# Optimization experiments

Hardware: AMD Instinct MI355X
Metric: run time of the kernel (lower is better)

## Reference

```python
import jax, jax.numpy as jnp
import numpy as np

B, S, H, I, E, TOP_K = 2, 2048, 768, 3072, 7, 2


def setup_inputs() -> dict:
    key = jax.random.key(0)
    ks = jax.random.split(key, 5)
    x = jax.random.normal(ks[0], (B, S, H), dtype=jnp.float32)
    # parameter init ~ torch Linear default scale (1/sqrt(fan_in))
    wg = jax.random.normal(ks[1], (H, E), dtype=jnp.float32) / np.sqrt(H)
    bg = jnp.zeros((E,), dtype=jnp.float32)
    w1 = jax.random.normal(ks[2], (E, H, I), dtype=jnp.float32) / np.sqrt(H)
    b1 = jnp.zeros((E, I), dtype=jnp.float32)
    w2 = jax.random.normal(ks[3], (E, I, H), dtype=jnp.float32) / np.sqrt(I)
    b2 = jnp.zeros((E, H), dtype=jnp.float32)
    return {"x": x, "wg": wg, "bg": bg, "w1": w1, "b1": b1, "w2": w2, "b2": b2}


def _gate_weights(gate_logits):
    # top-k mask: -inf everywhere except top-k slots, then softmax.
    # Equivalent: softmax over top-k values, scattered back into [.., E].
    vals, idx = jax.lax.top_k(gate_logits, TOP_K)           # [B,S,K]
    wk = jax.nn.softmax(vals, axis=-1)                       # [B,S,K]
    onehot = jax.nn.one_hot(idx, E, dtype=gate_logits.dtype)  # [B,S,K,E]
    return jnp.einsum('bsk,bske->bse', wk, onehot)           # [B,S,E]


def reference(x, wg, bg, w1, b1, w2, b2):
    gate_logits = jnp.einsum('bsh,he->bse', x, wg) + bg      # [B,S,E]
    gate_w = _gate_weights(gate_logits)                       # [B,S,E]
    # dense all-expert FFN (the module evaluates EVERY expert on every token)
    h = jnp.einsum('bsh,ehi->bsei', x, w1) + b1              # [B,S,E,I]
    h = jax.nn.gelu(h, approximate=False)                    # torch.nn.GELU (exact erf)
    expert_out = jnp.einsum('bsei,eih->bseh', h, w2) + b2    # [B,S,E,H]
    out = jnp.einsum('bseh,bse->bsh', expert_out, gate_w)    # weighted combine
    # dropout is identity in eval mode
    return (out, gate_w)
```

## Files before the change

### kernel.cpp

```cpp
#include <hip/hip_runtime.h>
#include <hip/hip_bf16.h>
#include <cmath>

#define NT 4096
#define HD 768
#define ID 3072
#define NE 7
#define NP 8192
#define TM 128
#define TN 128
#define BK 32
#define KS 2
#define NT2 (HD / TN)
#define SLOTS 384
#define NRING 3

using short8 = __attribute__((ext_vector_type(8))) short;
using f32x4  = __attribute__((ext_vector_type(4))) float;
typedef __hip_bfloat16 bf16;

typedef const __attribute__((address_space(1))) void* gas_ptr;
typedef __attribute__((address_space(3))) void* las_ptr;
#define GLDS(g, l) __builtin_amdgcn_global_load_lds((gas_ptr)(g), (las_ptr)(l), 16, 0, 0)

#define BAR()   asm volatile("s_barrier" ::: "memory")
#define WAITL() asm volatile("s_waitcnt lgkmcnt(0)" ::: "memory")
#define WV4()   asm volatile("s_waitcnt vmcnt(4)" ::: "memory")
#define WV0()   asm volatile("s_waitcnt vmcnt(0)" ::: "memory")
#define SCHEDB() __builtin_amdgcn_sched_barrier(0)

__device__ inline float b2f(unsigned short u) {
  unsigned v = (unsigned)u << 16; float f; __builtin_memcpy(&f, &v, 4); return f;
}

__device__ inline float gelu_erf(float v) {
  float xa = fabsf(v) * 0.70710678118654752f;
  float t  = __builtin_amdgcn_rcpf(1.0f + 0.3275911f * xa);
  float p  = t * (0.254829592f + t * (-0.284496736f + t * (1.421413741f +
             t * (-1.453152027f + t * 1.061405429f))));
  float er = 1.0f - p * __expf(-xa * xa);
  er = (v < 0.0f) ? -er : er;
  return 0.5f * v * (1.0f + er);
}

__global__ __launch_bounds__(64) void gate_kernel(
    const float* __restrict__ x, const float* __restrict__ wg, const float* __restrict__ bg,
    float* __restrict__ gate_out, bf16* __restrict__ xb,
    float* __restrict__ pair_w, int* __restrict__ tokexp)
{
  int t = blockIdx.x;
  int lane = threadIdx.x;
  const float* xr = x + (size_t)t * HD;
  float acc[NE];
#pragma unroll
  for (int e = 0; e < NE; e++) acc[e] = 0.f;
#pragma unroll
  for (int j = 0; j < HD / 64; j++) {
    int h = lane + j * 64;
    float xv = xr[h];
    xb[(size_t)t * HD + h] = __float2bfloat16(xv);
    const float* wr = wg + (size_t)h * NE;
#pragma unroll
    for (int e = 0; e < NE; e++) acc[e] += xv * wr[e];
  }
#pragma unroll
  for (int e = 0; e < NE; e++) {
    float v = acc[e];
    for (int s = 32; s > 0; s >>= 1) v += __shfl_down(v, s, 64);
    acc[e] = v;
  }
  if (lane == 0) {
    float lg[NE];
#pragma unroll
    for (int e = 0; e < NE; e++) lg[e] = acc[e] + bg[e];
    int i0 = 0;
    for (int e = 1; e < NE; e++) if (lg[e] > lg[i0]) i0 = e;
    int i1 = -1;
    for (int e = 0; e < NE; e++) {
      if (e == i0) continue;
      if (i1 < 0 || lg[e] > lg[i1]) i1 = e;
    }
    float v0 = lg[i0], v1 = lg[i1];
    float e1 = expf(v1 - v0);
    float inv = 1.f / (1.f + e1);
    float w0 = inv, w1v = e1 * inv;
    float* go = gate_out + (size_t)t * NE;
#pragma unroll
    for (int e = 0; e < NE; e++) go[e] = 0.f;
    go[i0] = w0; go[i1] = w1v;
    pair_w[2 * t + 0] = w0;
    pair_w[2 * t + 1] = w1v;
    tokexp[2 * t + 0] = i0;
    tokexp[2 * t + 1] = i1;
  }
}

__global__ __launch_bounds__(256) void route_kernel(
    const int* __restrict__ tokexp, int* __restrict__ elist, int* __restrict__ counts)
{
  __shared__ int wcnt[4];
  int e = blockIdx.x;
  int tid = threadIdx.x, wv = tid >> 6, ln = tid & 63;
  int base = 0;
  for (int chunk = 0; chunk < NP; chunk += 256) {
    int p = chunk + tid;
    bool m = (tokexp[p] == e);
    unsigned long long bal = __ballot(m);
    if (ln == 0) wcnt[wv] = __popcll(bal);
    __syncthreads();
    int pre = 0;
#pragma unroll
    for (int w = 0; w < 4; w++) pre += (w < wv) ? wcnt[w] : 0;
    int rank = pre + __popcll(bal & ((1ull << ln) - 1ull));
    if (m) elist[e * NP + base + rank] = p;
    base += wcnt[0] + wcnt[1] + wcnt[2] + wcnt[3];
    __syncthreads();
  }
  if (tid == 0) counts[e] = base;
}

__global__ __launch_bounds__(256) void transpose_cvt_kernel(
    const float* __restrict__ src, bf16* __restrict__ dst, int K, int N)
{
  __shared__ float tile[64][65];
  int e = blockIdx.z;
  int n0 = blockIdx.x * 64;
  int k0 = blockIdx.y * 64;
  const float* s = src + (size_t)e * K * N;
  bf16* d = dst + (size_t)e * K * N;
  int t = threadIdx.x;
  {
    int kk = t >> 4;
    int nc = (t & 15) << 2;
#pragma unroll
    for (int r = 0; r < 4; r++) {
      int k = kk + r * 16;
      float4 v = *(const float4*)(s + (size_t)(k0 + k) * N + n0 + nc);
      tile[k][nc + 0] = v.x; tile[k][nc + 1] = v.y;
      tile[k][nc + 2] = v.z; tile[k][nc + 3] = v.w;
    }
  }
  __syncthreads();
  {
    int c = t & 15;
    int nbase = t >> 4;
#pragma unroll
    for (int r = 0; r < 4; r++) {
      int n = nbase + r * 16;
      bf16 tmp[4];
#pragma unroll
      for (int i = 0; i < 4; i++) tmp[i] = __float2bfloat16(tile[4 * c + i][n]);
      ushort4 u; __builtin_memcpy(&u, tmp, 8);
      *(ushort4*)(d + (size_t)(n0 + n) * K + k0 + 4 * c) = u;
    }
  }
}


#define STAGE_TILE(As_, Bs_, a0_, a1_, bA_, bB_, t_, s_, c0_, c1_) do {          \
    bf16* dA_ = (bf16*)(As_) + (size_t)(s_) * TM * 32;                           \
    bf16* dB_ = (bf16*)(Bs_) + (size_t)(s_) * TN * 32;                           \
    GLDS((a0_) + (size_t)(t_) * BK, dA_ + (c0_) * 8);                            \
    GLDS((a1_) + (size_t)(t_) * BK, dA_ + (c1_) * 8);                            \
    GLDS((bA_) + (size_t)(t_) * BK, dB_ + (c0_) * 8);                            \
    GLDS((bB_) + (size_t)(t_) * BK, dB_ + (c1_) * 8);                            \
  } while (0)

__global__ __launch_bounds__(256) void ffn1_kernel(
    const bf16* __restrict__ xb, const bf16* __restrict__ w1t, const float* __restrict__ b1,
    const int* __restrict__ counts, const int* __restrict__ elist, bf16* __restrict__ hbuf)
{
  __shared__ bf16 As[NRING][TM][4][8];
  __shared__ bf16 Bs[NRING][TN][4][8];
  __shared__ int plist[TM];

  int tid = threadIdx.x;
  int e, base = 0, cnt = 0, acct = 0;
  bool found = false;
  for (e = 0; e < NE; e++) {
    cnt = counts[e];
    int tiles = (cnt + TM - 1) / TM;
    if ((int)blockIdx.y < acct + tiles) { base = ((int)blockIdx.y - acct) * TM; found = true; break; }
    acct += tiles;
  }
  if (!found) return;

  if (tid < TM) {
    int r = base + tid;
    plist[tid] = (r < cnt) ? elist[e * NP + r] : -1;
  }
  __syncthreads();

  const int n0 = blockIdx.x * TN;
  const bf16* Bsrc = w1t + (size_t)e * ID * HD;

  int c0 = tid, c1 = tid + 256;
  int r0 = c0 >> 2, p0 = c0 & 3, k0 = p0 ^ ((r0 >> 1) & 3);
  int r1 = c1 >> 2, p1 = c1 & 3, k1 = p1 ^ ((r1 >> 1) & 3);
  int pr0 = plist[r0], pr1 = plist[r1];
  const bf16* a0 = xb + (size_t)((pr0 >= 0 ? pr0 : 0) >> 1) * HD + k0 * 8;
  const bf16* a1 = xb + (size_t)((pr1 >= 0 ? pr1 : 0) >> 1) * HD + k1 * 8;
  const bf16* b0 = Bsrc + (size_t)(n0 + r0) * HD + k0 * 8;
  const bf16* b1v = Bsrc + (size_t)(n0 + r1) * HD + k1 * 8;

  int wave = tid >> 6, lane = tid & 63;
  int wm = (wave & 1) << 6, wn = (wave >> 1) << 6;
  int lr = lane & 15, quad = lane >> 4;
  int ph = quad ^ ((lr >> 1) & 3);

  f32x4 acc[4][4] = {};
  const int NIT = HD / BK;

  STAGE_TILE(As, Bs, a0, a1, b0, b1v, 0, 0, c0, c1);
  STAGE_TILE(As, Bs, a0, a1, b0, b1v, 1, 1, c0, c1);

  int sr = 0;
  for (int t = 0; t < NIT; ++t) {
    if (t < NIT - 1) { WV4(); } else { WV0(); }
    BAR();
    short8 af[4], bfr[4];
#pragma unroll
    for (int i = 0; i < 4; i++) af[i] = *(const short8*)&As[sr][wm + i * 16 + lr][ph][0];
#pragma unroll
    for (int j = 0; j < 4; j++) bfr[j] = *(const short8*)&Bs[sr][wn + j * 16 + lr][ph][0];
    if (t + 2 < NIT) {
      int sw = sr + 2; if (sw >= NRING) sw -= NRING;
      STAGE_TILE(As, Bs, a0, a1, b0, b1v, t + 2, sw, c0, c1);
    }
    WAITL(); SCHEDB();
    __builtin_amdgcn_s_setprio(1);
#pragma unroll
    for (int i = 0; i < 4; i++)
#pragma unroll
      for (int j = 0; j < 4; j++)
        acc[i][j] = __builtin_amdgcn_mfma_f32_16x16x32_bf16(af[i], bfr[j], acc[i][j], 0, 0, 0);
    __builtin_amdgcn_s_setprio(0);
    sr = (sr + 1 == NRING) ? 0 : sr + 1;
  }

  const float* b1e = b1 + (size_t)e * ID;
#pragma unroll
  for (int j = 0; j < 4; j++) {
    int col = n0 + wn + j * 16 + lr;
    float bias = b1e[col];
#pragma unroll
    for (int i = 0; i < 4; i++) {
#pragma unroll
      for (int r = 0; r < 4; r++) {
        int mrow = wm + i * 16 + quad * 4 + r;
        int p = plist[mrow];
        if (p >= 0) {
          float v = acc[i][j][r] + bias;
          hbuf[(size_t)p * ID + col] = __float2bfloat16(gelu_erf(v));
        }
      }
    }
  }
}

__global__ __launch_bounds__(256) void ffn2_kernel(
    const bf16* __restrict__ hbuf, const bf16* __restrict__ w2t, const float* __restrict__ b2,
    const int* __restrict__ counts, const int* __restrict__ elist,
    const float* __restrict__ pair_w, bf16* __restrict__ pout)
{
  __shared__ bf16 As[NRING][TM][4][8];
  __shared__ bf16 Bs[NRING][TN][4][8];
  __shared__ int plist[TM];

  int tid = threadIdx.x;
  int xcd = blockIdx.x;
  int slot = blockIdx.y;
  int e = 0, seg = 0, base = 0, cnt = 0, n0 = 0;
  bool found = false;
  for (int p = xcd; p < 2 * NE; p += 8) {
    int pe = p >> 1;
    int c = counts[pe];
    int tiles = ((c + TM - 1) / TM) * NT2;
    if (slot < tiles) {
      e = pe; seg = p & 1; cnt = c;
      base = (slot / NT2) * TM;
      n0 = (slot % NT2) * TN;
      found = true; break;
    }
    slot -= tiles;
  }
  if (!found) return;

  if (tid < TM) {
    int r = base + tid;
    plist[tid] = (r < cnt) ? elist[e * NP + r] : -1;
  }
  __syncthreads();

  const int kbase = seg * (ID / KS);
  const bf16* Bsrc = w2t + (size_t)e * HD * ID;

  int c0 = tid, c1 = tid + 256;
  int r0 = c0 >> 2, p0 = c0 & 3, k0 = p0 ^ ((r0 >> 1) & 3);
  int r1 = c1 >> 2, p1 = c1 & 3, k1 = p1 ^ ((r1 >> 1) & 3);
  int pr0 = plist[r0], pr1 = plist[r1];
  const bf16* a0 = hbuf + (size_t)(pr0 >= 0 ? pr0 : 0) * ID + kbase + k0 * 8;
  const bf16* a1 = hbuf + (size_t)(pr1 >= 0 ? pr1 : 0) * ID + kbase + k1 * 8;
  const bf16* b0 = Bsrc + (size_t)(n0 + r0) * ID + kbase + k0 * 8;
  const bf16* b1v = Bsrc + (size_t)(n0 + r1) * ID + kbase + k1 * 8;

  int wave = tid >> 6, lane = tid & 63;
  int wm = (wave & 1) << 6, wn = (wave >> 1) << 6;
  int lr = lane & 15, quad = lane >> 4;
  int ph = quad ^ ((lr >> 1) & 3);

  f32x4 acc[4][4] = {};
  const int NIT = (ID / KS) / BK;

  STAGE_TILE(As, Bs, a0, a1, b0, b1v, 0, 0, c0, c1);
  STAGE_TILE(As, Bs, a0, a1, b0, b1v, 1, 1, c0, c1);

  int sr = 0;
  for (int t = 0; t < NIT; ++t) {
    if (t < NIT - 1) { WV4(); } else { WV0(); }
    BAR();
    short8 af[4], bfr[4];
#pragma unroll
    for (int i = 0; i < 4; i++) af[i] = *(const short8*)&As[sr][wm + i * 16 + lr][ph][0];
#pragma unroll
    for (int j = 0; j < 4; j++) bfr[j] = *(const short8*)&Bs[sr][wn + j * 16 + lr][ph][0];
    if (t + 2 < NIT) {
      int sw = sr + 2; if (sw >= NRING) sw -= NRING;
      STAGE_TILE(As, Bs, a0, a1, b0, b1v, t + 2, sw, c0, c1);
    }
    WAITL(); SCHEDB();
    __builtin_amdgcn_s_setprio(1);
#pragma unroll
    for (int i = 0; i < 4; i++)
#pragma unroll
      for (int j = 0; j < 4; j++)
        acc[i][j] = __builtin_amdgcn_mfma_f32_16x16x32_bf16(af[i], bfr[j], acc[i][j], 0, 0, 0);
    __builtin_amdgcn_s_setprio(0);
    sr = (sr + 1 == NRING) ? 0 : sr + 1;
  }

  const float* b2e = b2 + (size_t)e * HD;
#pragma unroll
  for (int j = 0; j < 4; j++) {
    int col = n0 + wn + j * 16 + lr;
    float bias = (seg == 0) ? b2e[col] : 0.f;
#pragma unroll
    for (int i = 0; i < 4; i++) {
#pragma unroll
      for (int r = 0; r < 4; r++) {
        int mrow = wm + i * 16 + quad * 4 + r;
        int p = plist[mrow];
        if (p >= 0) {
          float v = (acc[i][j][r] + bias) * pair_w[p];
          pout[((size_t)seg * NP + p) * HD + col] = __float2bfloat16(v);
        }
      }
    }
  }
}

__global__ __launch_bounds__(192) void combine_kernel(
    const bf16* __restrict__ pout, float* __restrict__ out)
{
  int t = blockIdx.x, j = threadIdx.x;
  f32x4 o = {0.f, 0.f, 0.f, 0.f};
#pragma unroll
  for (int s = 0; s < KS; s++) {
#pragma unroll
    for (int k = 0; k < 2; k++) {
      const ushort4* v = (const ushort4*)(pout + ((size_t)s * NP + 2 * t + k) * HD);
      ushort4 u = v[j];
      o[0] += b2f(u.x); o[1] += b2f(u.y); o[2] += b2f(u.z); o[3] += b2f(u.w);
    }
  }
  ((f32x4*)(out + (size_t)t * HD))[j] = o;
}

extern "C" void kernel_launch(void* const* d_in, const int* in_sizes, int n_in,
                              void* d_out, int out_size, void* d_ws, size_t ws_size,
                              hipStream_t stream)
{
  const float* x  = (const float*)d_in[0];
  const float* wg = (const float*)d_in[1];
  const float* bg = (const float*)d_in[2];
  const float* w1 = (const float*)d_in[3];
  const float* b1 = (const float*)d_in[4];
  const float* w2 = (const float*)d_in[5];
  const float* b2 = (const float*)d_in[6];
  float* out = (float*)d_out;
  float* gate_out = out + (size_t)NT * HD;

  char* ws = (char*)d_ws;
  size_t off = 0;
  int* counts  = (int*)(ws + off);  off += 256;
  int* tokexp  = (int*)(ws + off);  off += (size_t)NP * 4;
  int* elist   = (int*)(ws + off);  off += (size_t)NE * NP * 4;
  float* pair_w = (float*)(ws + off); off += (size_t)NP * 4;
  bf16* xb   = (bf16*)(ws + off);   off += (size_t)NT * HD * 2;
  bf16* w1t  = (bf16*)(ws + off);   off += (size_t)NE * HD * ID * 2;
  bf16* w2t  = (bf16*)(ws + off);   off += (size_t)NE * HD * ID * 2;
  bf16* hbuf = (bf16*)(ws + off);   off += (size_t)NP * ID * 2;
  bf16* pout = (bf16*)(ws + off);   off += (size_t)KS * NP * HD * 2;

  gate_kernel<<<NT, 64, 0, stream>>>(x, wg, bg, gate_out, xb, pair_w, tokexp);
  route_kernel<<<NE, 256, 0, stream>>>(tokexp, elist, counts);
  transpose_cvt_kernel<<<dim3(ID / 64, HD / 64, NE), 256, 0, stream>>>(w1, w1t, HD, ID);
  transpose_cvt_kernel<<<dim3(HD / 64, ID / 64, NE), 256, 0, stream>>>(w2, w2t, ID, HD);
  ffn1_kernel<<<dim3(ID / TN, 71), 256, 0, stream>>>(xb, w1t, b1, counts, elist, hbuf);
  ffn2_kernel<<<dim3(8, SLOTS), 256, 0, stream>>>(hbuf, w2t, b2, counts, elist, pair_w, pout);
  combine_kernel<<<NT, 192, 0, stream>>>(pout, out);
}
```

Measured before the change: 370.2 us.

## Double M-tile to 256 with 512-thread blocks, XCD-aware grid swizzle, vectorized epilogue

Both grouped GEMM kernels now use 256-row token tiles with 8 waves per block, so each weight tile loaded into LDS is reused across twice as many tokens. FFN1 switches to a 1D grid remapped so consecutive blocks on the same XCD share weight columns, improving L2 locality. The MFMA operands are swapped so each lane holds 4 consecutive output columns, which lets the epilogue do one plist lookup per row and write vectorized 8-byte stores with float4 bias loads. The trade-offs are more registers and LDS per block, fewer resident blocks, and more padding waste on partial expert tiles.

Measured after the change: 338.6 us. -8.5%, faster.

```diff
diff --git a/kernel.cpp b/kernel.cpp
--- a/kernel.cpp
+++ b/kernel.cpp
@@ -7,13 +7,16 @@
 #define ID 3072
 #define NE 7
 #define NP 8192
-#define TM 128
+#define TM 256
 #define TN 128
 #define BK 32
 #define KS 2
 #define NT2 (HD / TN)
-#define SLOTS 384
+#define SLOTS 208
 #define NRING 3
+#define FFN1_MT 39
+#define FFN1_GRID (24 * FFN1_MT)
+#define FFN1_CPX (FFN1_GRID / 8)
 
 using short8 = __attribute__((ext_vector_type(8))) short;
 using f32x4  = __attribute__((ext_vector_type(4))) float;
@@ -25,7 +28,7 @@
 
 #define BAR()   asm volatile("s_barrier" ::: "memory")
 #define WAITL() asm volatile("s_waitcnt lgkmcnt(0)" ::: "memory")
-#define WV4()   asm volatile("s_waitcnt vmcnt(4)" ::: "memory")
+#define WV3()   asm volatile("s_waitcnt vmcnt(3)" ::: "memory")
 #define WV0()   asm volatile("s_waitcnt vmcnt(0)" ::: "memory")
 #define SCHEDB() __builtin_amdgcn_sched_barrier(0)
 
@@ -157,16 +160,7 @@
 }
 
 
-#define STAGE_TILE(As_, Bs_, a0_, a1_, bA_, bB_, t_, s_, c0_, c1_) do {          \
-    bf16* dA_ = (bf16*)(As_) + (size_t)(s_) * TM * 32;                           \
-    bf16* dB_ = (bf16*)(Bs_) + (size_t)(s_) * TN * 32;                           \
-    GLDS((a0_) + (size_t)(t_) * BK, dA_ + (c0_) * 8);                            \
-    GLDS((a1_) + (size_t)(t_) * BK, dA_ + (c1_) * 8);                            \
-    GLDS((bA_) + (size_t)(t_) * BK, dB_ + (c0_) * 8);                            \
-    GLDS((bB_) + (size_t)(t_) * BK, dB_ + (c1_) * 8);                            \
-  } while (0)
-
-__global__ __launch_bounds__(256) void ffn1_kernel(
+__global__ __launch_bounds__(512) void ffn1_kernel(
     const bf16* __restrict__ xb, const bf16* __restrict__ w1t, const float* __restrict__ b1,
     const int* __restrict__ counts, const int* __restrict__ elist, bf16* __restrict__ hbuf)
 {
@@ -175,12 +169,16 @@
   __shared__ int plist[TM];
 
   int tid = threadIdx.x;
+  int raw = blockIdx.x;
+  int v = (raw & 7) * FFN1_CPX + (raw >> 3);
+  int by = v / 24, bx = v % 24;
+
   int e, base = 0, cnt = 0, acct = 0;
   bool found = false;
   for (e = 0; e < NE; e++) {
     cnt = counts[e];
     int tiles = (cnt + TM - 1) / TM;
-    if ((int)blockIdx.y < acct + tiles) { base = ((int)blockIdx.y - acct) * TM; found = true; break; }
+    if (by < acct + tiles) { base = (by - acct) * TM; found = true; break; }
     acct += tiles;
   }
   if (!found) return;
@@ -191,32 +189,40 @@
   }
   __syncthreads();
 
-  const int n0 = blockIdx.x * TN;
+  const int n0 = bx * TN;
   const bf16* Bsrc = w1t + (size_t)e * ID * HD;
 
-  int c0 = tid, c1 = tid + 256;
-  int r0 = c0 >> 2, p0 = c0 & 3, k0 = p0 ^ ((r0 >> 1) & 3);
-  int r1 = c1 >> 2, p1 = c1 & 3, k1 = p1 ^ ((r1 >> 1) & 3);
+  int c0 = tid, c1 = tid + 512, cb = tid;
+  int r0 = c0 >> 2, k0 = (c0 & 3) ^ ((r0 >> 1) & 3);
+  int r1 = c1 >> 2, k1 = (c1 & 3) ^ ((r1 >> 1) & 3);
+  int rb = cb >> 2, kb = (cb & 3) ^ ((rb >> 1) & 3);
   int pr0 = plist[r0], pr1 = plist[r1];
   const bf16* a0 = xb + (size_t)((pr0 >= 0 ? pr0 : 0) >> 1) * HD + k0 * 8;
   const bf16* a1 = xb + (size_t)((pr1 >= 0 ? pr1 : 0) >> 1) * HD + k1 * 8;
-  const bf16* b0 = Bsrc + (size_t)(n0 + r0) * HD + k0 * 8;
-  const bf16* b1v = Bsrc + (size_t)(n0 + r1) * HD + k1 * 8;
+  const bf16* b0 = Bsrc + (size_t)(n0 + rb) * HD + kb * 8;
+
+#define STAGE1(t_, s_) do {                                                      \
+    bf16* dA_ = (bf16*)As + (size_t)(s_) * TM * 32;                              \
+    bf16* dB_ = (bf16*)Bs + (size_t)(s_) * TN * 32;                              \
+    GLDS(a0 + (size_t)(t_) * BK, dA_ + c0 * 8);                                  \
+    GLDS(a1 + (size_t)(t_) * BK, dA_ + c1 * 8);                                  \
+    GLDS(b0 + (size_t)(t_) * BK, dB_ + cb * 8);                                  \
+  } while (0)
 
   int wave = tid >> 6, lane = tid & 63;
-  int wm = (wave & 1) << 6, wn = (wave >> 1) << 6;
+  int wm = (wave >> 1) << 6, wn = (wave & 1) << 6;
   int lr = lane & 15, quad = lane >> 4;
   int ph = quad ^ ((lr >> 1) & 3);
 
   f32x4 acc[4][4] = {};
   const int NIT = HD / BK;
 
-  STAGE_TILE(As, Bs, a0, a1, b0, b1v, 0, 0, c0, c1);
-  STAGE_TILE(As, Bs, a0, a1, b0, b1v, 1, 1, c0, c1);
+  STAGE1(0, 0);
+  STAGE1(1, 1);
 
   int sr = 0;
   for (int t = 0; t < NIT; ++t) {
-    if (t < NIT - 1) { WV4(); } else { WV0(); }
+    if (t < NIT - 1) { WV3(); } else { WV0(); }
     BAR();
     short8 af[4], bfr[4];
 #pragma unroll
@@ -225,7 +231,7 @@
     for (int j = 0; j < 4; j++) bfr[j] = *(const short8*)&Bs[sr][wn + j * 16 + lr][ph][0];
     if (t + 2 < NIT) {
       int sw = sr + 2; if (sw >= NRING) sw -= NRING;
-      STAGE_TILE(As, Bs, a0, a1, b0, b1v, t + 2, sw, c0, c1);
+      STAGE1(t + 2, sw);
     }
     WAITL(); SCHEDB();
     __builtin_amdgcn_s_setprio(1);
@@ -233,32 +239,36 @@
     for (int i = 0; i < 4; i++)
 #pragma unroll
       for (int j = 0; j < 4; j++)
-        acc[i][j] = __builtin_amdgcn_mfma_f32_16x16x32_bf16(af[i], bfr[j], acc[i][j], 0, 0, 0);
+        acc[i][j] = __builtin_amdgcn_mfma_f32_16x16x32_bf16(bfr[j], af[i], acc[i][j], 0, 0, 0);
     __builtin_amdgcn_s_setprio(0);
     sr = (sr + 1 == NRING) ? 0 : sr + 1;
   }
+#undef STAGE1
 
   const float* b1e = b1 + (size_t)e * ID;
 #pragma unroll
-  for (int j = 0; j < 4; j++) {
-    int col = n0 + wn + j * 16 + lr;
-    float bias = b1e[col];
-#pragma unroll
-    for (int i = 0; i < 4; i++) {
-#pragma unroll
-      for (int r = 0; r < 4; r++) {
-        int mrow = wm + i * 16 + quad * 4 + r;
-        int p = plist[mrow];
-        if (p >= 0) {
-          float v = acc[i][j][r] + bias;
-          hbuf[(size_t)p * ID + col] = __float2bfloat16(gelu_erf(v));
-        }
+  for (int i = 0; i < 4; i++) {
+    int mrow = wm + i * 16 + lr;
+    int p = plist[mrow];
+    if (p >= 0) {
+      bf16* drow = hbuf + (size_t)p * ID;
+#pragma unroll
+      for (int j = 0; j < 4; j++) {
+        int colb = n0 + wn + j * 16 + (quad << 2);
+        float4 bs = *(const float4*)(b1e + colb);
+        bf16 o[4];
+        o[0] = __float2bfloat16(gelu_erf(acc[i][j][0] + bs.x));
+        o[1] = __float2bfloat16(gelu_erf(acc[i][j][1] + bs.y));
+        o[2] = __float2bfloat16(gelu_erf(acc[i][j][2] + bs.z));
+        o[3] = __float2bfloat16(gelu_erf(acc[i][j][3] + bs.w));
+        ushort4 u; __builtin_memcpy(&u, o, 8);
+        *(ushort4*)(drow + colb) = u;
       }
     }
   }
 }
 
-__global__ __launch_bounds__(256) void ffn2_kernel(
+__global__ __launch_bounds__(512) void ffn2_kernel(
     const bf16* __restrict__ hbuf, const bf16* __restrict__ w2t, const float* __restrict__ b2,
     const int* __restrict__ counts, const int* __restrict__ elist,
     const float* __restrict__ pair_w, bf16* __restrict__ pout)
@@ -295,29 +305,37 @@
   const int kbase = seg * (ID / KS);
   const bf16* Bsrc = w2t + (size_t)e * HD * ID;
 
-  int c0 = tid, c1 = tid + 256;
-  int r0 = c0 >> 2, p0 = c0 & 3, k0 = p0 ^ ((r0 >> 1) & 3);
-  int r1 = c1 >> 2, p1 = c1 & 3, k1 = p1 ^ ((r1 >> 1) & 3);
+  int c0 = tid, c1 = tid + 512, cb = tid;
+  int r0 = c0 >> 2, k0 = (c0 & 3) ^ ((r0 >> 1) & 3);
+  int r1 = c1 >> 2, k1 = (c1 & 3) ^ ((r1 >> 1) & 3);
+  int rb = cb >> 2, kb = (cb & 3) ^ ((rb >> 1) & 3);
   int pr0 = plist[r0], pr1 = plist[r1];
   const bf16* a0 = hbuf + (size_t)(pr0 >= 0 ? pr0 : 0) * ID + kbase + k0 * 8;
   const bf16* a1 = hbuf + (size_t)(pr1 >= 0 ? pr1 : 0) * ID + kbase + k1 * 8;
-  const bf16* b0 = Bsrc + (size_t)(n0 + r0) * ID + kbase + k0 * 8;
-  const bf16* b1v = Bsrc + (size_t)(n0 + r1) * ID + kbase + k1 * 8;
+  const bf16* b0 = Bsrc + (size_t)(n0 + rb) * ID + kbase + kb * 8;
+
+#define STAGE2(t_, s_) do {                                                      \
+    bf16* dA_ = (bf16*)As + (size_t)(s_) * TM * 32;                              \
+    bf16* dB_ = (bf16*)Bs + (size_t)(s_) * TN * 32;                              \
+    GLDS(a0 + (size_t)(t_) * BK, dA_ + c0 * 8);                                  \
+    GLDS(a1 + (size_t)(t_) * BK, dA_ + c1 * 8);                                  \
+    GLDS(b0 + (size_t)(t_) * BK, dB_ + cb * 8);                                  \
+  } while (0)
 
   int wave = tid >> 6, lane = tid & 63;
-  int wm = (wave & 1) << 6, wn = (wave >> 1) << 6;
+  int wm = (wave >> 1) << 6, wn = (wave & 1) << 6;
   int lr = lane & 15, quad = lane >> 4;
   int ph = quad ^ ((lr >> 1) & 3);
 
   f32x4 acc[4][4] = {};
   const int NIT = (ID / KS) / BK;
 
-  STAGE_TILE(As, Bs, a0, a1, b0, b1v, 0, 0, c0, c1);
-  STAGE_TILE(As, Bs, a0, a1, b0, b1v, 1, 1, c0, c1);
+  STAGE2(0, 0);
+  STAGE2(1, 1);
 
   int sr = 0;
   for (int t = 0; t < NIT; ++t) {
-    if (t < NIT - 1) { WV4(); } else { WV0(); }
+    if (t < NIT - 1) { WV3(); } else { WV0(); }
     BAR();
     short8 af[4], bfr[4];
 #pragma unroll
@@ -326,7 +344,7 @@
     for (int j = 0; j < 4; j++) bfr[j] = *(const short8*)&Bs[sr][wn + j * 16 + lr][ph][0];
     if (t + 2 < NIT) {
       int sw = sr + 2; if (sw >= NRING) sw -= NRING;
-      STAGE_TILE(As, Bs, a0, a1, b0, b1v, t + 2, sw, c0, c1);
+      STAGE2(t + 2, sw);
     }
     WAITL(); SCHEDB();
     __builtin_amdgcn_s_setprio(1);
@@ -334,26 +352,35 @@
     for (int i = 0; i < 4; i++)
 #pragma unroll
       for (int j = 0; j < 4; j++)
-        acc[i][j] = __builtin_amdgcn_mfma_f32_16x16x32_bf16(af[i], bfr[j], acc[i][j], 0, 0, 0);
+        acc[i][j] = __builtin_amdgcn_mfma_f32_16x16x32_bf16(bfr[j], af[i], acc[i][j], 0, 0, 0);
     __builtin_amdgcn_s_setprio(0);
     sr = (sr + 1 == NRING) ? 0 : sr + 1;
   }
+#undef STAGE2
 
   const float* b2e = b2 + (size_t)e * HD;
 #pragma unroll
-  for (int j = 0; j < 4; j++) {
-    int col = n0 + wn + j * 16 + lr;
-    float bias = (seg == 0) ? b2e[col] : 0.f;
-#pragma unroll
-    for (int i = 0; i < 4; i++) {
-#pragma unroll
-      for (int r = 0; r < 4; r++) {
-        int mrow = wm + i * 16 + quad * 4 + r;
-        int p = plist[mrow];
-        if (p >= 0) {
-          float v = (acc[i][j][r] + bias) * pair_w[p];
-          pout[((size_t)seg * NP + p) * HD + col] = __float2bfloat16(v);
+  for (int i = 0; i < 4; i++) {
+    int mrow = wm + i * 16 + lr;
+    int p = plist[mrow];
+    if (p >= 0) {
+      float pw = pair_w[p];
+      bf16* drow = pout + ((size_t)seg * NP + p) * HD;
+#pragma unroll
+      for (int j = 0; j < 4; j++) {
+        int colb = n0 + wn + j * 16 + (quad << 2);
+        float bx_ = 0.f, by_ = 0.f, bz_ = 0.f, bw_ = 0.f;
+        if (seg == 0) {
+          float4 bs = *(const float4*)(b2e + colb);
+          bx_ = bs.x; by_ = bs.y; bz_ = bs.z; bw_ = bs.w;
         }
+        bf16 o[4];
+        o[0] = __float2bfloat16((acc[i][j][0] + bx_) * pw);
+        o[1] = __float2bfloat16((acc[i][j][1] + by_) * pw);
+        o[2] = __float2bfloat16((acc[i][j][2] + bz_) * pw);
+        o[3] = __float2bfloat16((acc[i][j][3] + bw_) * pw);
+        ushort4 u; __builtin_memcpy(&u, o, 8);
+        *(ushort4*)(drow + colb) = u;
       }
     }
   }
@@ -406,7 +433,7 @@
   route_kernel<<<NE, 256, 0, stream>>>(tokexp, elist, counts);
   transpose_cvt_kernel<<<dim3(ID / 64, HD / 64, NE), 256, 0, stream>>>(w1, w1t, HD, ID);
   transpose_cvt_kernel<<<dim3(HD / 64, ID / 64, NE), 256, 0, stream>>>(w2, w2t, ID, HD);
-  ffn1_kernel<<<dim3(ID / TN, 71), 256, 0, stream>>>(xb, w1t, b1, counts, elist, hbuf);
-  ffn2_kernel<<<dim3(8, SLOTS), 256, 0, stream>>>(hbuf, w2t, b2, counts, elist, pair_w, pout);
+  ffn1_kernel<<<FFN1_GRID, 512, 0, stream>>>(xb, w1t, b1, counts, elist, hbuf);
+  ffn2_kernel<<<dim3(8, SLOTS), 512, 0, stream>>>(hbuf, w2t, b2, counts, elist, pair_w, pout);
   combine_kernel<<<NT, 192, 0, stream>>>(pout, out);
 }
```
